# Optimization experiments

Measured on AMD Instinct MI355X. Metric: run time of the kernel, lower is better.

## Reference

```python
import jax, jax.numpy as jnp
import numpy as np

B, L, V, D, NCTX, DEPTH, VD = 4096, 77, 49408, 512, 4, 9, 768


def setup_inputs() -> dict:
    key = jax.random.key(0)
    ks = jax.random.split(key, 8)
    text = jax.random.randint(ks[0], (B, L), 0, V, dtype=jnp.int32)
    emb = jax.random.normal(ks[1], (V, D), dtype=jnp.float32) * 0.02
    ctx = jax.random.normal(ks[2], (NCTX, D), dtype=jnp.float32) * 0.02
    proj_w = jax.random.normal(ks[3], (VD, D), dtype=jnp.float32) * (1.0 / np.sqrt(D))
    proj_b = jnp.zeros((VD,), dtype=jnp.float32)
    cpt = jax.random.normal(ks[4], (DEPTH - 1, NCTX, D), dtype=jnp.float32) * 0.02
    cw = jax.random.normal(ks[5], (DEPTH - 1, VD, D), dtype=jnp.float32) * (1.0 / np.sqrt(D))
    cb = jnp.zeros((DEPTH - 1, VD), dtype=jnp.float32)
    return {"text": text, "emb": emb, "ctx": ctx, "proj_w": proj_w,
            "proj_b": proj_b, "cpt": cpt, "cw": cw, "cb": cb}


def _construct_prompts(text, emb, ctx):
    # Vectorized version of the per-token python loop in construct_prompts.
    b, l = text.shape
    n_ctx = ctx.shape[0]
    trunc = l - n_ctx - 1  # 77 - n_ctx - 1 tokens of the original sentence kept
    pt = jnp.zeros((b, l), dtype=text.dtype)
    pt = pt.at[:, 0].set(text[:, 0])                       # BOS
    pt = pt.at[:, n_ctx + 1:].set(text[:, 1:1 + trunc])    # shifted sentence
    # if the last slot is non-zero, replace with token at argmax position (EOT)
    ind = jnp.argmax(text, axis=-1)
    eot = jnp.take_along_axis(text, ind[:, None], axis=1)[:, 0]
    last = pt[:, -1]
    pt = pt.at[:, -1].set(jnp.where(last != 0, eot, last))
    # embedding gather, then scatter learned ctx into slots 1..1+n_ctx
    pe = emb[pt]  # [B, 77, D]
    pe = pe.at[:, 1:1 + n_ctx, :].set(jnp.broadcast_to(ctx, (b, n_ctx, ctx.shape[1])))
    return pe, pt.astype(jnp.float32)


def reference(text, emb, ctx, proj_w, proj_b, cpt, cw, cb):
    pe, pt = _construct_prompts(text, emb, ctx)
    proj_ctx = ctx @ proj_w.T + proj_b                      # [n_ctx, 768]
    vdp = jnp.einsum('knd,kod->kno', cpt, cw) + cb[:, None, :]  # [depth-1, n_ctx, 768]
    return (pe, pt, ctx, proj_ctx, cpt, vdp)
```

## Files before the change

### kernel.cpp

```cpp
#include <hip/hip_runtime.h>
#include <hip/hip_bf16.h>

#define BB   4096
#define LL   77
#define DD   512
#define NCTX 4
#define KK   8
#define VD   768

#define OFF_PE   0L
#define OFF_PT   161480704L
#define OFF_CTX  161796096L
#define OFF_PROJ 161798144L
#define OFF_CPT  161801216L
#define OFF_VDP  161817600L

typedef float f32x4 __attribute__((ext_vector_type(4)));

#define DOT_BLOCKS 6912
#define PT_BLOCKS  1024
#define CPY_BLOCKS 18

__global__ __launch_bounds__(256) void k_prep(const int* __restrict__ text,
                                              const float* __restrict__ ctx,
                                              const float* __restrict__ proj_w,
                                              const float* __restrict__ proj_b,
                                              const float* __restrict__ cpt,
                                              const float* __restrict__ cw,
                                              const float* __restrict__ cb,
                                              float* __restrict__ out) {
    int blk = blockIdx.x;
    int tid = threadIdx.x;

    if (blk < DOT_BLOCKS) {
        int gid  = blk * 256 + tid;
        int wave = gid >> 6;
        int lane = gid & 63;

        const float* a;
        const float* b;
        float bias;
        float* dst;

        if (wave < NCTX * VD) {
            int n = wave / VD;
            int o = wave - n * VD;
            a    = ctx + n * DD;
            b    = proj_w + (long)o * DD;
            bias = proj_b[o];
            dst  = out + OFF_PROJ + wave;
        } else {
            int w = wave - NCTX * VD;
            int k = w / (NCTX * VD);
            int r = w - k * (NCTX * VD);
            int n = r / VD;
            int o = r - n * VD;
            a    = cpt + (long)(k * NCTX + n) * DD;
            b    = cw + (long)(k * VD + o) * DD;
            bias = cb[k * VD + o];
            dst  = out + OFF_VDP + w;
        }

        const f32x4* a4 = (const f32x4*)a + lane * 2;
        const f32x4* b4 = (const f32x4*)b + lane * 2;
        f32x4 x0 = a4[0], x1 = a4[1];
        f32x4 y0 = b4[0], y1 = b4[1];
        float s = x0.x * y0.x + x0.y * y0.y + x0.z * y0.z + x0.w * y0.w
                + x1.x * y1.x + x1.y * y1.y + x1.z * y1.z + x1.w * y1.w;
        #pragma unroll
        for (int off = 32; off; off >>= 1) s += __shfl_xor(s, off);
        if (lane == 0) *dst = s + bias;

    } else if (blk < DOT_BLOCKS + PT_BLOCKS) {
        int gid  = (blk - DOT_BLOCKS) * 256 + tid;
        int row  = gid >> 6;
        int lane = gid & 63;
        const int* t = text + row * LL;

        const int NEG = -2147483647 - 1;
        int v0 = (lane < LL)      ? t[lane]      : NEG;
        int v1 = (lane + 64 < LL) ? t[lane + 64] : NEG;
        int m  = v0 > v1 ? v0 : v1;
        #pragma unroll
        for (int off = 32; off; off >>= 1) {
            int o = __shfl_xor(m, off);
            m = o > m ? o : m;
        }

        float* dst = out + OFF_PT + (long)row * LL;
        #pragma unroll
        for (int pass = 0; pass < 2; ++pass) {
            int pos = lane + pass * 64;
            if (pos < LL) {
                int v;
                if (pos == 0)          v = t[0];
                else if (pos <= NCTX)  v = 0;
                else if (pos == LL - 1){ int x = t[LL - 5]; v = (x != 0) ? m : 0; }
                else                   v = t[pos - NCTX];
                dst[pos] = (float)v;
            }
        }

    } else {
        int i = (blk - DOT_BLOCKS - PT_BLOCKS) * 256 + tid;
        const f32x4* c4  = (const f32x4*)ctx;
        const f32x4* p4  = (const f32x4*)cpt;
        f32x4* o4 = (f32x4*)out;
        if (i < 512) {
            o4[OFF_CTX / 4 + i] = c4[i];
        } else {
            o4[OFF_CPT / 4 + (i - 512)] = p4[i - 512];
        }
    }
}

__global__ __launch_bounds__(256) void k_gather(const f32x4* __restrict__ emb,
                                                const f32x4* __restrict__ ctx,
                                                const float* __restrict__ pt_f,
                                                f32x4* __restrict__ pe) {
    int t    = blockIdx.x * 256 + threadIdx.x;
    int row  = t >> 6;
    int lane = t & 63;
    int pos  = row % LL;

    const f32x4* src;
    if (pos >= 1 && pos <= NCTX) {
        src = ctx + (pos - 1) * (DD / 4);
    } else {
        int tok = (int)pt_f[row];
        src = emb + (long)tok * (DD / 4);
    }
    f32x4 a = src[lane];
    f32x4 b = src[lane + 64];
    f32x4* dst = pe + (long)row * (DD / 4);
    __builtin_nontemporal_store(a, dst + lane);
    __builtin_nontemporal_store(b, dst + lane + 64);
}

extern "C" void kernel_launch(void* const* d_in, const int* in_sizes, int n_in,
                              void* d_out, int out_size, void* d_ws, size_t ws_size,
                              hipStream_t stream) {
    const int*   text   = (const int*)d_in[0];
    const float* emb    = (const float*)d_in[1];
    const float* ctx    = (const float*)d_in[2];
    const float* proj_w = (const float*)d_in[3];
    const float* proj_b = (const float*)d_in[4];
    const float* cpt    = (const float*)d_in[5];
    const float* cw     = (const float*)d_in[6];
    const float* cb     = (const float*)d_in[7];
    float* out = (float*)d_out;

    k_prep<<<DOT_BLOCKS + PT_BLOCKS + CPY_BLOCKS, 256, 0, stream>>>(
        text, ctx, proj_w, proj_b, cpt, cw, cb, out);

    {
        long threads = (long)BB * LL * 64;
        int  blocks  = (int)(threads / 256);
        k_gather<<<blocks, 256, 0, stream>>>((const f32x4*)emb,
                                             (const f32x4*)ctx,
                                             out + OFF_PT,
                                             (f32x4*)(out + OFF_PE));
    }
}
```

Before: 758.8 us.

## Fuse token construction and embedding gather into one per-row kernel

Merges the prompt-token construction and the embedding gather into a single kernel where each block handles one batch row. The block computes the row's argmax and tokens, writes the float token row, and stores per-position source pointers in shared memory. All 256 threads then stream the row's embedding data out with nontemporal stores. This drops the second launch and the round trip of re-reading the float token ids from global memory, at the cost of two block barriers and fewer, larger blocks for the gather.

```diff
diff --git a/kernel.cpp b/kernel.cpp
--- a/kernel.cpp
+++ b/kernel.cpp
@@ -1,5 +1,6 @@
 #include <hip/hip_runtime.h>
 #include <hip/hip_bf16.h>
+#include <stdint.h>
 
 #define BB   4096
 #define LL   77
@@ -18,10 +19,11 @@
 typedef float f32x4 __attribute__((ext_vector_type(4)));
 
 #define DOT_BLOCKS 6912
-#define PT_BLOCKS  1024
 #define CPY_BLOCKS 18
+#define ROW_F4     (LL * DD / 4)
 
-__global__ __launch_bounds__(256) void k_prep(const int* __restrict__ text,
+__global__ __launch_bounds__(256) void k_main(const int* __restrict__ text,
+                                              const float* __restrict__ emb,
                                               const float* __restrict__ ctx,
                                               const float* __restrict__ proj_w,
                                               const float* __restrict__ proj_b,
@@ -32,8 +34,50 @@
     int blk = blockIdx.x;
     int tid = threadIdx.x;
 
-    if (blk < DOT_BLOCKS) {
-        int gid  = blk * 256 + tid;
+    if (blk < BB) {
+        __shared__ uintptr_t srcp[LL];
+        __shared__ int smax;
+        const int* t = text + blk * LL;
+
+        if (tid < 64) {
+            int v0 = (tid < LL) ? t[tid] : 0;
+            int v1 = (tid + 64 < LL) ? t[tid + 64] : 0;
+            int m = v0 > v1 ? v0 : v1;
+            #pragma unroll
+            for (int off = 32; off; off >>= 1) {
+                int o = __shfl_xor(m, off);
+                m = o > m ? o : m;
+            }
+            if (tid == 0) smax = m;
+        }
+        __syncthreads();
+
+        if (tid < LL) {
+            int v;
+            if (tid == 0)           v = t[0];
+            else if (tid <= NCTX)   v = 0;
+            else if (tid == LL - 1) { int x = t[LL - 5]; v = (x != 0) ? smax : 0; }
+            else                    v = t[tid - NCTX];
+
+            const float* s;
+            if (tid >= 1 && tid <= NCTX) s = ctx + (tid - 1) * DD;
+            else                         s = emb + (long)v * DD;
+            srcp[tid] = (uintptr_t)s;
+            out[OFF_PT + (long)blk * LL + tid] = (float)v;
+        }
+        __syncthreads();
+
+        f32x4* dst = (f32x4*)out + (long)blk * ROW_F4;
+        #pragma unroll 4
+        for (int i = tid; i < ROW_F4; i += 256) {
+            int p = i >> 7;
+            int c = i & 127;
+            const f32x4* s = (const f32x4*)srcp[p];
+            __builtin_nontemporal_store(s[c], dst + i);
+        }
+
+    } else if (blk < BB + DOT_BLOCKS) {
+        int gid  = (blk - BB) * 256 + tid;
         int wave = gid >> 6;
         int lane = gid & 63;
 
@@ -71,40 +115,10 @@
         for (int off = 32; off; off >>= 1) s += __shfl_xor(s, off);
         if (lane == 0) *dst = s + bias;
 
-    } else if (blk < DOT_BLOCKS + PT_BLOCKS) {
-        int gid  = (blk - DOT_BLOCKS) * 256 + tid;
-        int row  = gid >> 6;
-        int lane = gid & 63;
-        const int* t = text + row * LL;
-
-        const int NEG = -2147483647 - 1;
-        int v0 = (lane < LL)      ? t[lane]      : NEG;
-        int v1 = (lane + 64 < LL) ? t[lane + 64] : NEG;
-        int m  = v0 > v1 ? v0 : v1;
-        #pragma unroll
-        for (int off = 32; off; off >>= 1) {
-            int o = __shfl_xor(m, off);
-            m = o > m ? o : m;
-        }
-
-        float* dst = out + OFF_PT + (long)row * LL;
-        #pragma unroll
-        for (int pass = 0; pass < 2; ++pass) {
-            int pos = lane + pass * 64;
-            if (pos < LL) {
-                int v;
-                if (pos == 0)          v = t[0];
-                else if (pos <= NCTX)  v = 0;
-                else if (pos == LL - 1){ int x = t[LL - 5]; v = (x != 0) ? m : 0; }
-                else                   v = t[pos - NCTX];
-                dst[pos] = (float)v;
-            }
-        }
-
     } else {
-        int i = (blk - DOT_BLOCKS - PT_BLOCKS) * 256 + tid;
-        const f32x4* c4  = (const f32x4*)ctx;
-        const f32x4* p4  = (const f32x4*)cpt;
+        int i = (blk - BB - DOT_BLOCKS) * 256 + tid;
+        const f32x4* c4 = (const f32x4*)ctx;
+        const f32x4* p4 = (const f32x4*)cpt;
         f32x4* o4 = (f32x4*)out;
         if (i < 512) {
             o4[OFF_CTX / 4 + i] = c4[i];
@@ -112,29 +126,6 @@
             o4[OFF_CPT / 4 + (i - 512)] = p4[i - 512];
         }
     }
-}
-
-__global__ __launch_bounds__(256) void k_gather(const f32x4* __restrict__ emb,
-                                                const f32x4* __restrict__ ctx,
-                                                const float* __restrict__ pt_f,
-                                                f32x4* __restrict__ pe) {
-    int t    = blockIdx.x * 256 + threadIdx.x;
-    int row  = t >> 6;
-    int lane = t & 63;
-    int pos  = row % LL;
-
-    const f32x4* src;
-    if (pos >= 1 && pos <= NCTX) {
-        src = ctx + (pos - 1) * (DD / 4);
-    } else {
-        int tok = (int)pt_f[row];
-        src = emb + (long)tok * (DD / 4);
-    }
-    f32x4 a = src[lane];
-    f32x4 b = src[lane + 64];
-    f32x4* dst = pe + (long)row * (DD / 4);
-    __builtin_nontemporal_store(a, dst + lane);
-    __builtin_nontemporal_store(b, dst + lane + 64);
 }
 
 extern "C" void kernel_launch(void* const* d_in, const int* in_sizes, int n_in,
@@ -150,15 +141,6 @@
     const float* cb     = (const float*)d_in[7];
     float* out = (float*)d_out;
 
-    k_prep<<<DOT_BLOCKS + PT_BLOCKS + CPY_BLOCKS, 256, 0, stream>>>(
-        text, ctx, proj_w, proj_b, cpt, cw, cb, out);
-
-    {
-        long threads = (long)BB * LL * 64;
-        int  blocks  = (int)(threads / 256);
-        k_gather<<<blocks, 256, 0, stream>>>((const f32x4*)emb,
-                                             (const f32x4*)ctx,
-                                             out + OFF_PT,
-                                             (f32x4*)(out + OFF_PE));
-    }
+    k_main<<<BB + DOT_BLOCKS + CPY_BLOCKS, 256, 0, stream>>>(
+        text, emb, ctx, proj_w, proj_b, cpt, cw, cb, out);
 }
```

Measured after the change: 763.4 us. About the same (+0.6%).

## Deduplicate embedding gather via token histogram, scan, and bucketed scatter

Applied to the files above, without the earlier changes.

Replaces the per-row embedding gather with a counting-sort pipeline. A histogram of token ids is built with atomics, prefix-scanned in a single block, and each row position is scattered into per-token buckets. Each vocabulary row is then read once and written to every output position that uses it, while the ctx slots are written by broadcast blocks in the prep kernel. This cuts redundant embedding reads, but adds a memset, three extra launches, a serial single-block scan, heavy global atomics, and scattered non-coalesced writes with load imbalance on frequent tokens.

```diff
diff --git a/kernel.cpp b/kernel.cpp
--- a/kernel.cpp
+++ b/kernel.cpp
@@ -1,8 +1,10 @@
 #include <hip/hip_runtime.h>
 #include <hip/hip_bf16.h>
+#include <stdint.h>
 
 #define BB   4096
 #define LL   77
+#define VV   49408
 #define DD   512
 #define NCTX 4
 #define KK   8
@@ -17,18 +19,25 @@
 
 typedef float f32x4 __attribute__((ext_vector_type(4)));
 
-#define DOT_BLOCKS 6912
-#define PT_BLOCKS  1024
-#define CPY_BLOCKS 18
-
-__global__ __launch_bounds__(256) void k_prep(const int* __restrict__ text,
-                                              const float* __restrict__ ctx,
-                                              const float* __restrict__ proj_w,
-                                              const float* __restrict__ proj_b,
-                                              const float* __restrict__ cpt,
-                                              const float* __restrict__ cw,
-                                              const float* __restrict__ cb,
-                                              float* __restrict__ out) {
+#define NEMB      73
+#define TOKSTRIDE 128
+#define VPAD      49664
+
+#define DOT_BLOCKS   6912
+#define PT_BLOCKS    1024
+#define CPY_BLOCKS   18
+#define BCAST_BLOCKS 8192
+
+__global__ __launch_bounds__(256) void k_prep_hist(const int* __restrict__ text,
+                                                   const float* __restrict__ ctx,
+                                                   const float* __restrict__ proj_w,
+                                                   const float* __restrict__ proj_b,
+                                                   const float* __restrict__ cpt,
+                                                   const float* __restrict__ cw,
+                                                   const float* __restrict__ cb,
+                                                   float* __restrict__ out,
+                                                   int* __restrict__ cnt,
+                                                   int* __restrict__ tok) {
     int blk = blockIdx.x;
     int tid = threadIdx.x;
 
@@ -77,64 +86,134 @@
         int lane = gid & 63;
         const int* t = text + row * LL;
 
-        const int NEG = -2147483647 - 1;
-        int v0 = (lane < LL)      ? t[lane]      : NEG;
-        int v1 = (lane + 64 < LL) ? t[lane + 64] : NEG;
-        int m  = v0 > v1 ? v0 : v1;
+        int v0 = (lane < LL) ? t[lane] : 0;
+        int v1 = (lane + 64 < LL) ? t[lane + 64] : 0;
+        int m = v0 > v1 ? v0 : v1;
         #pragma unroll
         for (int off = 32; off; off >>= 1) {
             int o = __shfl_xor(m, off);
             m = o > m ? o : m;
         }
 
-        float* dst = out + OFF_PT + (long)row * LL;
+        float* pt_dst = out + OFF_PT + (long)row * LL;
+        int*   trow   = tok + (long)row * TOKSTRIDE;
         #pragma unroll
         for (int pass = 0; pass < 2; ++pass) {
             int pos = lane + pass * 64;
             if (pos < LL) {
                 int v;
-                if (pos == 0)          v = t[0];
-                else if (pos <= NCTX)  v = 0;
-                else if (pos == LL - 1){ int x = t[LL - 5]; v = (x != 0) ? m : 0; }
-                else                   v = t[pos - NCTX];
-                dst[pos] = (float)v;
+                if (pos == 0)           v = t[0];
+                else if (pos <= NCTX)   v = 0;
+                else if (pos == LL - 1) { int x = t[LL - 5]; v = (x != 0) ? m : 0; }
+                else                    v = t[pos - NCTX];
+                pt_dst[pos] = (float)v;
+                if (pos == 0 || pos > NCTX) {
+                    int e = (pos == 0) ? 0 : pos - NCTX;
+                    trow[e] = v;
+                    atomicAdd(&cnt[v], 1);
+                }
             }
         }
 
-    } else {
+    } else if (blk < DOT_BLOCKS + PT_BLOCKS + CPY_BLOCKS) {
         int i = (blk - DOT_BLOCKS - PT_BLOCKS) * 256 + tid;
-        const f32x4* c4  = (const f32x4*)ctx;
-        const f32x4* p4  = (const f32x4*)cpt;
+        const f32x4* c4 = (const f32x4*)ctx;
+        const f32x4* p4 = (const f32x4*)cpt;
         f32x4* o4 = (f32x4*)out;
         if (i < 512) {
             o4[OFF_CTX / 4 + i] = c4[i];
         } else {
             o4[OFF_CPT / 4 + (i - 512)] = p4[i - 512];
         }
-    }
-}
-
-__global__ __launch_bounds__(256) void k_gather(const f32x4* __restrict__ emb,
-                                                const f32x4* __restrict__ ctx,
-                                                const float* __restrict__ pt_f,
-                                                f32x4* __restrict__ pe) {
-    int t    = blockIdx.x * 256 + threadIdx.x;
-    int row  = t >> 6;
-    int lane = t & 63;
-    int pos  = row % LL;
-
-    const f32x4* src;
-    if (pos >= 1 && pos <= NCTX) {
-        src = ctx + (pos - 1) * (DD / 4);
+
     } else {
-        int tok = (int)pt_f[row];
-        src = emb + (long)tok * (DD / 4);
-    }
-    f32x4 a = src[lane];
-    f32x4 b = src[lane + 64];
-    f32x4* dst = pe + (long)row * (DD / 4);
-    __builtin_nontemporal_store(a, dst + lane);
-    __builtin_nontemporal_store(b, dst + lane + 64);
+        int g = (blk - DOT_BLOCKS - PT_BLOCKS - CPY_BLOCKS) * 256 + tid;
+        int b = g >> 9;
+        int j = (g >> 7) & 3;
+        int c = g & 127;
+        const f32x4* c4 = (const f32x4*)ctx;
+        f32x4* pe4 = (f32x4*)out;
+        __builtin_nontemporal_store(c4[j * 128 + c],
+                                    pe4 + ((long)b * LL + 1 + j) * 128 + c);
+    }
+}
+
+#define SCAN_T 1024
+#define CHUNK  49
+__global__ __launch_bounds__(SCAN_T) void k_scan(const int* __restrict__ cnt,
+                                                 int* __restrict__ off,
+                                                 int* __restrict__ cur) {
+    __shared__ int sdata[SCAN_T];
+    int tid  = threadIdx.x;
+    int base = tid * CHUNK;
+
+    int lsum = 0;
+    #pragma unroll 4
+    for (int k = 0; k < CHUNK; ++k) {
+        int i = base + k;
+        if (i < VV) lsum += cnt[i];
+    }
+    sdata[tid] = lsum;
+    __syncthreads();
+    for (int d = 1; d < SCAN_T; d <<= 1) {
+        int v = (tid >= d) ? sdata[tid - d] : 0;
+        __syncthreads();
+        sdata[tid] += v;
+        __syncthreads();
+    }
+    int run = sdata[tid] - lsum;
+    #pragma unroll 4
+    for (int k = 0; k < CHUNK; ++k) {
+        int i = base + k;
+        if (i < VV) {
+            off[i] = run;
+            cur[i] = run;
+            run += cnt[i];
+        }
+    }
+}
+
+__global__ __launch_bounds__(256) void k_scatter(const int* __restrict__ tok,
+                                                 int* __restrict__ cur,
+                                                 int* __restrict__ pairs) {
+    int g = blockIdx.x * 256 + threadIdx.x;
+    int r = g >> 7;
+    int e = g & 127;
+    if (e < NEMB) {
+        int v   = tok[(long)r * TOKSTRIDE + e];
+        int pos = (e == 0) ? 0 : e + NCTX;
+        int idx = atomicAdd(&cur[v], 1);
+        pairs[idx] = r * LL + pos;
+    }
+}
+
+__global__ __launch_bounds__(256) void k_gather_dedup(const f32x4* __restrict__ emb,
+                                                      const int* __restrict__ off,
+                                                      const int* __restrict__ cnt,
+                                                      const int* __restrict__ pairs,
+                                                      f32x4* __restrict__ pe) {
+    int gid  = blockIdx.x * 256 + threadIdx.x;
+    int t    = gid >> 6;
+    int lane = gid & 63;
+
+    int n = cnt[t];
+    if (n == 0) return;
+    int o = off[t];
+
+    const f32x4* er = emb + (long)t * 128 + lane * 2;
+    f32x4 r0 = er[0];
+    f32x4 r1 = er[1];
+
+    for (int base = 0; base < n; base += 64) {
+        int mcnt = n - base; if (mcnt > 64) mcnt = 64;
+        int flat = (lane < mcnt) ? pairs[o + base + lane] : 0;
+        for (int j = 0; j < mcnt; ++j) {
+            int f = __shfl(flat, j);
+            f32x4* d = pe + (long)f * 128 + lane * 2;
+            __builtin_nontemporal_store(r0, d);
+            __builtin_nontemporal_store(r1, d + 1);
+        }
+    }
 }
 
 extern "C" void kernel_launch(void* const* d_in, const int* in_sizes, int n_in,
@@ -150,15 +229,22 @@
     const float* cb     = (const float*)d_in[7];
     float* out = (float*)d_out;
 
-    k_prep<<<DOT_BLOCKS + PT_BLOCKS + CPY_BLOCKS, 256, 0, stream>>>(
-        text, ctx, proj_w, proj_b, cpt, cw, cb, out);
-
-    {
-        long threads = (long)BB * LL * 64;
-        int  blocks  = (int)(threads / 256);
-        k_gather<<<blocks, 256, 0, stream>>>((const f32x4*)emb,
-                                             (const f32x4*)ctx,
-                                             out + OFF_PT,
-                                             (f32x4*)(out + OFF_PE));
-    }
-}
+    int* cnt   = (int*)d_ws;
+    int* off   = cnt + VPAD;
+    int* cur   = off + VPAD;
+    int* tok   = cur + VPAD;
+    int* pairs = tok + (long)BB * TOKSTRIDE;
+
+    hipMemsetAsync(cnt, 0, VV * sizeof(int), stream);
+
+    k_prep_hist<<<DOT_BLOCKS + PT_BLOCKS + CPY_BLOCKS + BCAST_BLOCKS, 256, 0,
+                  stream>>>(text, ctx, proj_w, proj_b, cpt, cw, cb, out, cnt, tok);
+
+    k_scan<<<1, SCAN_T, 0, stream>>>(cnt, off, cur);
+
+    k_scatter<<<BB * 128 / 256, 256, 0, stream>>>(tok, cur, pairs);
+
+    k_gather_dedup<<<VV * 64 / 256, 256, 0, stream>>>((const f32x4*)emb,
+                                                      off, cnt, pairs,
+                                                      (f32x4*)(out + OFF_PE));
+}
```

Measured after the change: 998.1 us. 31.5% more time.
